# Optimization experiments

Measured on AMD Instinct MI355X. Metric: run time of the kernel, lower is better.

The kernel has to match this reference:

```python
import jax, jax.numpy as jnp
import numpy as np

D_FEATURE = 1024
HEAD = 16
D_K = 64
D_V = 64
EPS = 1e-6


def setup_inputs() -> dict:
    key = jax.random.key(0)
    ks = jax.random.split(key, 12)
    B, S = 2, 2048
    s_in = 1.0 / np.sqrt(D_FEATURE)
    s_o = 1.0 / np.sqrt(HEAD * D_V)
    return {
        "q": jax.random.normal(ks[0], (B, S, D_FEATURE), jnp.float32),
        "k": jax.random.normal(ks[1], (B, S, D_FEATURE), jnp.float32),
        "v": jax.random.normal(ks[2], (B, S, D_FEATURE), jnp.float32),
        "Wq": jax.random.uniform(ks[3], (D_FEATURE, HEAD * D_K), jnp.float32, -s_in, s_in),
        "bq": jnp.zeros((HEAD * D_K,), jnp.float32),
        "Wk": jax.random.uniform(ks[4], (D_FEATURE, HEAD * D_K), jnp.float32, -s_in, s_in),
        "bk": jnp.zeros((HEAD * D_K,), jnp.float32),
        "Wv": jax.random.uniform(ks[5], (D_FEATURE, HEAD * D_V), jnp.float32, -s_in, s_in),
        "bv": jnp.zeros((HEAD * D_V,), jnp.float32),
        "Wo": jax.random.uniform(ks[6], (HEAD * D_V, D_FEATURE), jnp.float32, -s_o, s_o),
        "bo": jnp.zeros((D_FEATURE,), jnp.float32),
        "gamma": jnp.ones((D_FEATURE,), jnp.float32),
        "beta": jnp.zeros((D_FEATURE,), jnp.float32),
    }


def reference(q, k, v, Wq, bq, Wk, bk, Wv, bv, Wo, bo, gamma, beta):
    B, Sq, _ = q.shape
    Sk, Sv = k.shape[1], v.shape[1]
    shortcut = v
    # projections -> (b, h, s, d)
    qh = (q @ Wq + bq).reshape(B, Sq, HEAD, D_K).transpose(0, 2, 1, 3)
    kh = (k @ Wk + bk).reshape(B, Sk, HEAD, D_K).transpose(0, 2, 1, 3)
    vh = (v @ Wv + bv).reshape(B, Sv, HEAD, D_V).transpose(0, 2, 1, 3)
    scale = 1.0 / np.sqrt(D_K).astype(np.float32)
    scores = jnp.einsum('bhqd,bhkd->bhqk', qh * scale, kh)
    attn = jax.nn.softmax(scores, axis=-1)  # dropout is identity (p=0 / eval)
    ctx = jnp.einsum('bhqk,bhkd->bhqd', attn, vh)
    ctx = ctx.transpose(0, 2, 1, 3).reshape(B, Sv, HEAD * D_V)
    out = ctx @ Wo + bo
    out = out + shortcut
    # LayerNorm, eps=1e-6
    mu = out.mean(-1, keepdims=True)
    var = out.var(-1, keepdims=True)
    out = (out - mu) * jax.lax.rsqrt(var + EPS) * gamma + beta
    return out
```

## Files before the change

### kernel.cpp

```cpp
#include <hip/hip_runtime.h>

#define D_FEAT 1024
#define NTOK   4096
#define SEQ    2048
#define NHEAD  16
#define DK     64
#define QSCALE 0.1803368801111204f

typedef float          f32x4  __attribute__((ext_vector_type(4)));
typedef float          f32x16 __attribute__((ext_vector_type(16)));
typedef short          s16x8  __attribute__((ext_vector_type(8)));
typedef unsigned short u16x4  __attribute__((ext_vector_type(4)));

__device__ __forceinline__ unsigned short f2bf(float f) {
  union { float f; unsigned int u; } x; x.f = f;
  unsigned int r = x.u + 0x7fffu + ((x.u >> 16) & 1u);
  return (unsigned short)(r >> 16);
}

__device__ __forceinline__ f32x4 mfma16(s16x8 a, s16x8 b, f32x4 c) {
  return __builtin_amdgcn_mfma_f32_16x16x32_bf16(a, b, c, 0, 0, 0);
}
__device__ __forceinline__ f32x16 mfma32(s16x8 a, s16x8 b, f32x16 c) {
  return __builtin_amdgcn_mfma_f32_32x32x16_bf16(a, b, c, 0, 0, 0);
}

__device__ __forceinline__ void gload16(const void* g, void* l) {
  __builtin_amdgcn_global_load_lds(
      (const __attribute__((address_space(1))) void*)g,
      (__attribute__((address_space(3))) void*)l, 16, 0, 0);
}

__global__ __launch_bounds__(256) void cast_bf16_kernel(
    const float* __restrict__ q, const float* __restrict__ k, const float* __restrict__ v,
    unsigned short* __restrict__ qb, unsigned short* __restrict__ kb, unsigned short* __restrict__ vb)
{
  int sel = blockIdx.y;
  const float* src = sel == 0 ? q : (sel == 1 ? k : v);
  unsigned short* dst = sel == 0 ? qb : (sel == 1 ? kb : vb);
  size_t i = ((size_t)blockIdx.x * 256 + threadIdx.x) * 4;
  float4 f = *(const float4*)(src + i);
  u16x4 o; o.x = f2bf(f.x); o.y = f2bf(f.y); o.z = f2bf(f.z); o.w = f2bf(f.w);
  *(u16x4*)(dst + i) = o;
}

__global__ __launch_bounds__(256) void transpose_cast_kernel(
    const float* __restrict__ W0, const float* __restrict__ W1,
    const float* __restrict__ W2, const float* __restrict__ W3,
    unsigned short* __restrict__ WT, unsigned short* __restrict__ Wot)
{
  __shared__ float tile[32][33];
  int z = blockIdx.z;
  const float* W = z == 0 ? W0 : z == 1 ? W1 : z == 2 ? W2 : W3;
  unsigned short* T = (z < 3) ? (WT + (size_t)z * 1024 * 1024) : Wot;
  int tx = threadIdx.x, ty = threadIdx.y;
  int n = blockIdx.x * 32 + tx;
  for (int i = 0; i < 4; ++i) {
    int k = blockIdx.y * 32 + ty + i * 8;
    tile[ty + i * 8][tx] = W[(size_t)k * D_FEAT + n];
  }
  __syncthreads();
  int k = blockIdx.y * 32 + tx;
  for (int i = 0; i < 4; ++i) {
    int n2 = blockIdx.x * 32 + ty + i * 8;
    T[(size_t)n2 * D_FEAT + k] = f2bf(tile[tx][ty + i * 8]);
  }
}

__global__ __launch_bounds__(256) void gemm_qkv(
    const unsigned short* __restrict__ qb, const unsigned short* __restrict__ kb,
    const unsigned short* __restrict__ vb, const unsigned short* __restrict__ WT,
    const float* __restrict__ bq, const float* __restrict__ bk, const float* __restrict__ bv,
    unsigned short* __restrict__ Qp, unsigned short* __restrict__ Kp, unsigned short* __restrict__ Vt)
{
  __shared__ __align__(16) unsigned short sA[128 * 32];
  __shared__ __align__(16) unsigned short sB[128 * 32];
  const int tid = threadIdx.x;
  const int wave = tid >> 6, lane = tid & 63;
  const int quad = lane >> 4, l16 = lane & 15;
  const int wx = wave & 1, wy = wave >> 1;
  const int bx = blockIdx.x;
  const int chunk = bx >> 3;

  const unsigned short* rA;
  const unsigned short* rB;
  int m0, n0;
  if (chunk < 2) {
    m0 = blockIdx.y * 128; n0 = (bx & 7) * 128;
    rA = (chunk ? kb : qb) + (size_t)m0 * D_FEAT;
    rB = WT + (size_t)(chunk * 1024 + n0) * D_FEAT;
  } else {
    m0 = (bx & 7) * 128; n0 = blockIdx.y * 128;
    rA = WT + (size_t)(2048 + m0) * D_FEAT;
    rB = vb + (size_t)n0 * D_FEAT;
  }

  f32x4 acc[4][4];
  for (int mt = 0; mt < 4; ++mt)
    for (int nt = 0; nt < 4; ++nt) acc[mt][nt] = (f32x4){0.f, 0.f, 0.f, 0.f};

  const int rw = lane >> 2;
  const int cl = (((lane & 3) ^ ((lane >> 3) & 3))) * 8;
  const int g0 = (quad ^ ((l16 >> 1) & 3)) * 8;

  for (int k0 = 0; k0 < D_FEAT; k0 += 32) {
    __syncthreads();
    for (int j = 0; j < 2; ++j) {
      int ch = wave * 2 + j;
      gload16(rA + (size_t)(ch * 16 + rw) * D_FEAT + k0 + cl, sA + ch * 512);
      gload16(rB + (size_t)(ch * 16 + rw) * D_FEAT + k0 + cl, sB + ch * 512);
    }
    __syncthreads();
    s16x8 af[4], bfr[4];
    for (int mt = 0; mt < 4; ++mt)
      af[mt] = *(const s16x8*)(sA + (wy * 64 + mt * 16 + l16) * 32 + g0);
    for (int nt = 0; nt < 4; ++nt)
      bfr[nt] = *(const s16x8*)(sB + (wx * 64 + nt * 16 + l16) * 32 + g0);
    for (int mt = 0; mt < 4; ++mt)
      for (int nt = 0; nt < 4; ++nt)
        acc[mt][nt] = mfma16(af[mt], bfr[nt], acc[mt][nt]);
  }

  if (chunk < 2) {
    const float* bias = chunk ? bk : bq;
    unsigned short* Cp = chunk ? Kp : Qp;
    const float scale = chunk == 0 ? QSCALE : 1.0f;
    for (int mt = 0; mt < 4; ++mt)
      for (int nt = 0; nt < 4; ++nt) {
        int col = n0 + wx * 64 + nt * 16 + l16;
        float bcol = bias[col];
        for (int r = 0; r < 4; ++r) {
          int row = m0 + wy * 64 + mt * 16 + quad * 4 + r;
          Cp[(size_t)row * D_FEAT + col] = f2bf((acc[mt][nt][r] + bcol) * scale);
        }
      }
  } else {
    for (int mt = 0; mt < 4; ++mt) {
      float bfeat[4];
      for (int r = 0; r < 4; ++r)
        bfeat[r] = bv[m0 + wy * 64 + mt * 16 + quad * 4 + r];
      for (int nt = 0; nt < 4; ++nt) {
        int n = n0 + wx * 64 + nt * 16 + l16;
        int b = n >> 11, tok = n & 2047;
        for (int r = 0; r < 4; ++r) {
          int f = m0 + wy * 64 + mt * 16 + quad * 4 + r;
          int h = f >> 6, dv = f & 63;
          Vt[(((size_t)(b * 16 + h) * 64 + dv) * SEQ) + tok] =
              f2bf(acc[mt][nt][r] + bfeat[r]);
        }
      }
    }
  }
}

__global__ __launch_bounds__(256) void gemm_o(
    const unsigned short* __restrict__ A, const unsigned short* __restrict__ Bt,
    const float* __restrict__ bias, const float* __restrict__ resid,
    float* __restrict__ Cout)
{
  __shared__ __align__(16) unsigned short sA[128 * 32];
  __shared__ __align__(16) unsigned short sB[64 * 32];
  const int tid = threadIdx.x;
  const int wave = tid >> 6, lane = tid & 63;
  const int quad = lane >> 4, l16 = lane & 15;
  const int wx = wave & 1, wy = wave >> 1;
  const int n0 = blockIdx.x * 64, m0 = blockIdx.y * 128;

  f32x4 acc[4][2];
  for (int mt = 0; mt < 4; ++mt)
    for (int nt = 0; nt < 2; ++nt) acc[mt][nt] = (f32x4){0.f, 0.f, 0.f, 0.f};

  const int rw = lane >> 2;
  const int cl = (((lane & 3) ^ ((lane >> 3) & 3))) * 8;
  const int g0 = (quad ^ ((l16 >> 1) & 3)) * 8;

  for (int k0 = 0; k0 < D_FEAT; k0 += 32) {
    __syncthreads();
    for (int j = 0; j < 2; ++j) {
      int ch = wave * 2 + j;
      gload16(A + (size_t)(m0 + ch * 16 + rw) * D_FEAT + k0 + cl, sA + ch * 512);
    }
    gload16(Bt + (size_t)(n0 + wave * 16 + rw) * D_FEAT + k0 + cl, sB + wave * 512);
    __syncthreads();
    s16x8 af[4], bfr[2];
    for (int mt = 0; mt < 4; ++mt)
      af[mt] = *(const s16x8*)(sA + (wy * 64 + mt * 16 + l16) * 32 + g0);
    for (int nt = 0; nt < 2; ++nt)
      bfr[nt] = *(const s16x8*)(sB + (wx * 32 + nt * 16 + l16) * 32 + g0);
    for (int mt = 0; mt < 4; ++mt)
      for (int nt = 0; nt < 2; ++nt)
        acc[mt][nt] = mfma16(af[mt], bfr[nt], acc[mt][nt]);
  }

  for (int mt = 0; mt < 4; ++mt)
    for (int nt = 0; nt < 2; ++nt) {
      int col = n0 + wx * 32 + nt * 16 + l16;
      float bcol = bias[col];
      for (int r = 0; r < 4; ++r) {
        int row = m0 + wy * 64 + mt * 16 + quad * 4 + r;
        Cout[(size_t)row * D_FEAT + col] =
            acc[mt][nt][r] + bcol + resid[(size_t)row * D_FEAT + col];
      }
    }
}

__global__ __launch_bounds__(256, 2) void flash_kernel(
    const unsigned short* __restrict__ Qp,
    const unsigned short* __restrict__ Kp,
    const unsigned short* __restrict__ Vt,
    unsigned short* __restrict__ ctx)
{
  __shared__ __align__(16) unsigned short sQ[128 * 64];
  __shared__ __align__(16) unsigned short sK[64 * 64];
  __shared__ __align__(16) unsigned short sV[64 * 64];

  const int tid = threadIdx.x;
  const int wave = tid >> 6, lane = tid & 63;
  const int l32 = lane & 31, h = lane >> 5;
  const int q0 = blockIdx.x * 128;
  const int bh = blockIdx.y, b = bh >> 4, hd = bh & 15;
  const size_t base = (size_t)b * SEQ * D_FEAT + (size_t)hd * DK;
  const unsigned short* vt = Vt + (size_t)bh * 64 * SEQ;

  const int rw8 = lane >> 3;
  const int cls = ((lane & 7) ^ (lane >> 3)) * 8;

  for (int j = 0; j < 4; ++j) {
    int ch = wave * 4 + j;
    gload16(Qp + base + (size_t)(q0 + ch * 8 + rw8) * D_FEAT + cls, sQ + ch * 512);
  }
  __syncthreads();

  const int qrow = wave * 32 + l32;
  const int qsw = qrow & 7;
  s16x8 bq[4];
  for (int s = 0; s < 4; ++s)
    bq[s] = *(const s16x8*)(sQ + qrow * 64 + ((2 * s + h) ^ qsw) * 8);

  unsigned short* sP = sQ;

  f32x16 o0, o1;
  for (int r = 0; r < 16; ++r) { o0[r] = 0.f; o1[r] = 0.f; }
  float m_i = -INFINITY, l_i = 0.f;

  const int ksw0 = l32 & 7;

  for (int k0 = 0; k0 < SEQ; k0 += 64) {
    __syncthreads();
    for (int j = 0; j < 2; ++j) {
      int ch = wave * 2 + j;
      gload16(Kp + base + (size_t)(k0 + ch * 8 + rw8) * D_FEAT + cls, sK + ch * 512);
      gload16(vt + (size_t)(ch * 8 + rw8) * SEQ + k0 + cls, sV + ch * 512);
    }
    __syncthreads();

    f32x16 st0, st1;
    for (int r = 0; r < 16; ++r) { st0[r] = 0.f; st1[r] = 0.f; }
    for (int s = 0; s < 4; ++s) {
      int csw = ((2 * s + h) ^ ksw0) * 8;
      s16x8 a0 = *(const s16x8*)(sK + l32 * 64 + csw);
      s16x8 a1 = *(const s16x8*)(sK + (32 + l32) * 64 + csw);
      st0 = mfma32(a0, bq[s], st0);
      st1 = mfma32(a1, bq[s], st1);
    }

    float mx = st0[0];
    for (int r = 0; r < 16; ++r) { mx = fmaxf(mx, st0[r]); mx = fmaxf(mx, st1[r]); }
    mx = fmaxf(mx, __shfl_xor(mx, 32, 64));
    float mn = fmaxf(m_i, mx);
    float alpha = __builtin_exp2f(m_i - mn);
    m_i = mn;

    float sum = 0.f;
    const int rowb = qrow * 64;
    for (int g = 0; g < 4; ++g) {
      unsigned int u[4];
      for (int r = 0; r < 4; ++r) {
        union { float f; unsigned int v; } x;
        x.f = __builtin_exp2f(st0[4 * g + r] - mn);
        sum += x.f; u[r] = x.v;
      }
      unsigned int w0 = __builtin_amdgcn_perm(u[1], u[0], 0x07060302u);
      unsigned int w1 = __builtin_amdgcn_perm(u[3], u[2], 0x07060302u);
      *(uint2*)(sP + rowb + ((g ^ qsw) * 8) + 4 * h) = make_uint2(w0, w1);
    }
    for (int g = 0; g < 4; ++g) {
      unsigned int u[4];
      for (int r = 0; r < 4; ++r) {
        union { float f; unsigned int v; } x;
        x.f = __builtin_exp2f(st1[4 * g + r] - mn);
        sum += x.f; u[r] = x.v;
      }
      unsigned int w0 = __builtin_amdgcn_perm(u[1], u[0], 0x07060302u);
      unsigned int w1 = __builtin_amdgcn_perm(u[3], u[2], 0x07060302u);
      *(uint2*)(sP + rowb + (((4 + g) ^ qsw) * 8) + 4 * h) = make_uint2(w0, w1);
    }
    sum += __shfl_xor(sum, 32, 64);
    l_i = l_i * alpha + sum;

    for (int r = 0; r < 16; ++r) { o0[r] *= alpha; o1[r] *= alpha; }

    s16x8 bp[4];
    for (int s = 0; s < 4; ++s)
      bp[s] = *(const s16x8*)(sP + rowb + ((2 * s + h) ^ qsw) * 8);

    for (int s = 0; s < 4; ++s) {
      int csw = ((2 * s + h) ^ ksw0) * 8;
      s16x8 a0 = *(const s16x8*)(sV + l32 * 64 + csw);
      s16x8 a1 = *(const s16x8*)(sV + (32 + l32) * 64 + csw);
      o0 = mfma32(a0, bp[s], o0);
      o1 = mfma32(a1, bp[s], o1);
    }
  }

  float inv = __builtin_amdgcn_rcpf(l_i);
  unsigned short* crow = ctx + base + (size_t)(q0 + qrow) * D_FEAT;
  for (int g = 0; g < 4; ++g) {
    u16x4 ov;
    for (int r = 0; r < 4; ++r) ov[r] = f2bf(o0[4 * g + r] * inv);
    *(u16x4*)(crow + 8 * g + 4 * h) = ov;
  }
  for (int g = 0; g < 4; ++g) {
    u16x4 ov;
    for (int r = 0; r < 4; ++r) ov[r] = f2bf(o1[4 * g + r] * inv);
    *(u16x4*)(crow + 32 + 8 * g + 4 * h) = ov;
  }
}

__global__ __launch_bounds__(256) void ln_kernel(
    const float* __restrict__ x, const float* __restrict__ gamma,
    const float* __restrict__ beta, float* __restrict__ out)
{
  const int row = blockIdx.x, tid = threadIdx.x;
  const int wave = tid >> 6, lane = tid & 63;
  const float* xr = x + (size_t)row * D_FEAT;
  float4 v = ((const float4*)xr)[tid];
  float s  = v.x + v.y + v.z + v.w;
  float ss = v.x * v.x + v.y * v.y + v.z * v.z + v.w * v.w;
  for (int off = 1; off < 64; off <<= 1) {
    s  += __shfl_xor(s,  off, 64);
    ss += __shfl_xor(ss, off, 64);
  }
  __shared__ float red[8];
  if (lane == 0) { red[wave] = s; red[wave + 4] = ss; }
  __syncthreads();
  s  = red[0] + red[1] + red[2] + red[3];
  ss = red[4] + red[5] + red[6] + red[7];
  float mean = s * (1.f / D_FEAT);
  float var  = ss * (1.f / D_FEAT) - mean * mean;
  float rstd = rsqrtf(var + 1e-6f);
  float4 g  = ((const float4*)gamma)[tid];
  float4 bt = ((const float4*)beta)[tid];
  float4 o;
  o.x = (v.x - mean) * rstd * g.x + bt.x;
  o.y = (v.y - mean) * rstd * g.y + bt.y;
  o.z = (v.z - mean) * rstd * g.z + bt.z;
  o.w = (v.w - mean) * rstd * g.w + bt.w;
  ((float4*)(out + (size_t)row * D_FEAT))[tid] = o;
}

extern "C" void kernel_launch(void* const* d_in, const int* in_sizes, int n_in,
                              void* d_out, int out_size, void* d_ws, size_t ws_size,
                              hipStream_t stream) {
  const float* q     = (const float*)d_in[0];
  const float* k     = (const float*)d_in[1];
  const float* v     = (const float*)d_in[2];
  const float* Wq    = (const float*)d_in[3];
  const float* bq    = (const float*)d_in[4];
  const float* Wk    = (const float*)d_in[5];
  const float* bk    = (const float*)d_in[6];
  const float* Wv    = (const float*)d_in[7];
  const float* bv    = (const float*)d_in[8];
  const float* Wo    = (const float*)d_in[9];
  const float* bo    = (const float*)d_in[10];
  const float* gamma = (const float*)d_in[11];
  const float* beta  = (const float*)d_in[12];

  char* w = (char*)d_ws;
  const size_t MB = 1u << 20;
  unsigned short* qb  = (unsigned short*)(w + 0 * MB);
  unsigned short* kb  = (unsigned short*)(w + 8 * MB);
  unsigned short* vb  = (unsigned short*)(w + 16 * MB);
  unsigned short* WT  = (unsigned short*)(w + 24 * MB);
  unsigned short* Wot = (unsigned short*)(w + 30 * MB);
  unsigned short* Qp  = (unsigned short*)(w + 32 * MB);
  unsigned short* Kp  = (unsigned short*)(w + 40 * MB);
  unsigned short* Vt  = (unsigned short*)(w + 48 * MB);
  unsigned short* ctx = (unsigned short*)(w + 56 * MB);
  float*          tmp = (float*)(w + 64 * MB);

  cast_bf16_kernel<<<dim3(4096, 3), 256, 0, stream>>>(q, k, v, qb, kb, vb);
  transpose_cast_kernel<<<dim3(32, 32, 4), dim3(32, 8), 0, stream>>>(
      Wq, Wk, Wv, Wo, WT, Wot);

  gemm_qkv<<<dim3(24, 32), 256, 0, stream>>>(qb, kb, vb, WT, bq, bk, bv, Qp, Kp, Vt);

  flash_kernel<<<dim3(SEQ / 128, 32), 256, 0, stream>>>(Qp, Kp, Vt, ctx);

  gemm_o<<<dim3(16, 32), 256, 0, stream>>>(ctx, Wot, bo, v, tmp);

  ln_kernel<<<NTOK, 256, 0, stream>>>(tmp, gamma, beta, (float*)d_out);
}
```

Measured before the change: 278.4 us.

## Split attention over key halves, merge prep kernels, widen GEMM K-tile

Several changes land together. The two preprocessing kernels are merged into one launch. Both GEMMs now use a 64-wide K tile with a new swizzle. The V projection epilogue transposes through LDS so it can write Vt with vectorized stores. Attention is split into two key-range halves per query block, which writes fp16 partial outputs plus max and sum statistics, and a new combine kernel merges them into ctx. The split doubles the flash grid for occupancy at the cost of an extra kernel and extra partial-output traffic; fp16 partials risk precision loss.

```diff
diff --git a/kernel.cpp b/kernel.cpp
--- a/kernel.cpp
+++ b/kernel.cpp
@@ -17,6 +17,12 @@
   unsigned int r = x.u + 0x7fffu + ((x.u >> 16) & 1u);
   return (unsigned short)(r >> 16);
 }
+__device__ __forceinline__ unsigned short f2h(float f) {
+  union { _Float16 h; unsigned short u; } x; x.h = (_Float16)f; return x.u;
+}
+__device__ __forceinline__ float h2f(unsigned short u) {
+  union { _Float16 h; unsigned short u; } x; x.u = u; return (float)x.h;
+}
 
 __device__ __forceinline__ f32x4 mfma16(s16x8 a, s16x8 b, f32x4 c) {
   return __builtin_amdgcn_mfma_f32_16x16x32_bf16(a, b, c, 0, 0, 0);
@@ -31,50 +37,54 @@
       (__attribute__((address_space(3))) void*)l, 16, 0, 0);
 }
 
-__global__ __launch_bounds__(256) void cast_bf16_kernel(
+__global__ __launch_bounds__(256) void prep_kernel(
     const float* __restrict__ q, const float* __restrict__ k, const float* __restrict__ v,
-    unsigned short* __restrict__ qb, unsigned short* __restrict__ kb, unsigned short* __restrict__ vb)
-{
-  int sel = blockIdx.y;
-  const float* src = sel == 0 ? q : (sel == 1 ? k : v);
-  unsigned short* dst = sel == 0 ? qb : (sel == 1 ? kb : vb);
-  size_t i = ((size_t)blockIdx.x * 256 + threadIdx.x) * 4;
-  float4 f = *(const float4*)(src + i);
-  u16x4 o; o.x = f2bf(f.x); o.y = f2bf(f.y); o.z = f2bf(f.z); o.w = f2bf(f.w);
-  *(u16x4*)(dst + i) = o;
-}
-
-__global__ __launch_bounds__(256) void transpose_cast_kernel(
-    const float* __restrict__ W0, const float* __restrict__ W1,
-    const float* __restrict__ W2, const float* __restrict__ W3,
+    const float* __restrict__ Wq, const float* __restrict__ Wk,
+    const float* __restrict__ Wv, const float* __restrict__ Wo,
+    unsigned short* __restrict__ qb, unsigned short* __restrict__ kb,
+    unsigned short* __restrict__ vb,
     unsigned short* __restrict__ WT, unsigned short* __restrict__ Wot)
 {
   __shared__ float tile[32][33];
-  int z = blockIdx.z;
-  const float* W = z == 0 ? W0 : z == 1 ? W1 : z == 2 ? W2 : W3;
-  unsigned short* T = (z < 3) ? (WT + (size_t)z * 1024 * 1024) : Wot;
-  int tx = threadIdx.x, ty = threadIdx.y;
-  int n = blockIdx.x * 32 + tx;
-  for (int i = 0; i < 4; ++i) {
-    int k = blockIdx.y * 32 + ty + i * 8;
-    tile[ty + i * 8][tx] = W[(size_t)k * D_FEAT + n];
-  }
-  __syncthreads();
-  int k = blockIdx.y * 32 + tx;
-  for (int i = 0; i < 4; ++i) {
-    int n2 = blockIdx.x * 32 + ty + i * 8;
-    T[(size_t)n2 * D_FEAT + k] = f2bf(tile[tx][ty + i * 8]);
-  }
-}
-
-__global__ __launch_bounds__(256) void gemm_qkv(
+  const int bx = blockIdx.x, tid = threadIdx.x;
+  if (bx < 12288) {
+    int sel = bx >> 12;
+    const float* src = sel == 0 ? q : (sel == 1 ? k : v);
+    unsigned short* dst = sel == 0 ? qb : (sel == 1 ? kb : vb);
+    size_t i = ((size_t)(bx & 4095) * 256 + tid) * 4;
+    float4 f = *(const float4*)(src + i);
+    u16x4 o; o.x = f2bf(f.x); o.y = f2bf(f.y); o.z = f2bf(f.z); o.w = f2bf(f.w);
+    *(u16x4*)(dst + i) = o;
+  } else {
+    int t = bx - 12288;
+    int z = t >> 10, rest = t & 1023;
+    int bxt = rest & 31, byt = rest >> 5;
+    const float* W = z == 0 ? Wq : z == 1 ? Wk : z == 2 ? Wv : Wo;
+    unsigned short* T = (z < 3) ? (WT + (size_t)z * 1024 * 1024) : Wot;
+    int tx = tid & 31, ty = tid >> 5;
+    int n = bxt * 32 + tx;
+    for (int i = 0; i < 4; ++i) {
+      int kk = byt * 32 + ty + i * 8;
+      tile[ty + i * 8][tx] = W[(size_t)kk * D_FEAT + n];
+    }
+    __syncthreads();
+    int kk = byt * 32 + tx;
+    for (int i = 0; i < 4; ++i) {
+      int n2 = bxt * 32 + ty + i * 8;
+      T[(size_t)n2 * D_FEAT + kk] = f2bf(tile[tx][ty + i * 8]);
+    }
+  }
+}
+
+__global__ __launch_bounds__(256, 3) void gemm_qkv(
     const unsigned short* __restrict__ qb, const unsigned short* __restrict__ kb,
     const unsigned short* __restrict__ vb, const unsigned short* __restrict__ WT,
     const float* __restrict__ bq, const float* __restrict__ bk, const float* __restrict__ bv,
     unsigned short* __restrict__ Qp, unsigned short* __restrict__ Kp, unsigned short* __restrict__ Vt)
 {
-  __shared__ __align__(16) unsigned short sA[128 * 32];
-  __shared__ __align__(16) unsigned short sB[128 * 32];
+  __shared__ __align__(16) unsigned short sAB[2 * 128 * 64];
+  unsigned short* sA = sAB;
+  unsigned short* sB = sAB + 128 * 64;
   const int tid = threadIdx.x;
   const int wave = tid >> 6, lane = tid & 63;
   const int quad = lane >> 4, l16 = lane & 15;
@@ -99,26 +109,30 @@
   for (int mt = 0; mt < 4; ++mt)
     for (int nt = 0; nt < 4; ++nt) acc[mt][nt] = (f32x4){0.f, 0.f, 0.f, 0.f};
 
-  const int rw = lane >> 2;
-  const int cl = (((lane & 3) ^ ((lane >> 3) & 3))) * 8;
-  const int g0 = (quad ^ ((l16 >> 1) & 3)) * 8;
-
-  for (int k0 = 0; k0 < D_FEAT; k0 += 32) {
-    __syncthreads();
-    for (int j = 0; j < 2; ++j) {
-      int ch = wave * 2 + j;
-      gload16(rA + (size_t)(ch * 16 + rw) * D_FEAT + k0 + cl, sA + ch * 512);
-      gload16(rB + (size_t)(ch * 16 + rw) * D_FEAT + k0 + cl, sB + ch * 512);
-    }
-    __syncthreads();
-    s16x8 af[4], bfr[4];
-    for (int mt = 0; mt < 4; ++mt)
-      af[mt] = *(const s16x8*)(sA + (wy * 64 + mt * 16 + l16) * 32 + g0);
-    for (int nt = 0; nt < 4; ++nt)
-      bfr[nt] = *(const s16x8*)(sB + (wx * 64 + nt * 16 + l16) * 32 + g0);
-    for (int mt = 0; mt < 4; ++mt)
+  const int rw8 = lane >> 3;
+  const int cls = ((lane & 7) ^ (lane >> 3)) * 8;
+  const int sw = l16 & 7;
+
+  for (int k0 = 0; k0 < D_FEAT; k0 += 64) {
+    __syncthreads();
+    for (int j = 0; j < 4; ++j) {
+      int ch = wave * 4 + j;
+      gload16(rA + (size_t)(ch * 8 + rw8) * D_FEAT + k0 + cls, sA + ch * 512);
+      gload16(rB + (size_t)(ch * 8 + rw8) * D_FEAT + k0 + cls, sB + ch * 512);
+    }
+    __syncthreads();
+    s16x8 af[2][4], bfr[2][4];
+    for (int kk = 0; kk < 2; ++kk) {
+      int c = ((kk * 4 + quad) ^ sw) * 8;
+      for (int mt = 0; mt < 4; ++mt)
+        af[kk][mt] = *(const s16x8*)(sA + (wy * 64 + mt * 16 + l16) * 64 + c);
       for (int nt = 0; nt < 4; ++nt)
-        acc[mt][nt] = mfma16(af[mt], bfr[nt], acc[mt][nt]);
+        bfr[kk][nt] = *(const s16x8*)(sB + (wx * 64 + nt * 16 + l16) * 64 + c);
+    }
+    for (int kk = 0; kk < 2; ++kk)
+      for (int mt = 0; mt < 4; ++mt)
+        for (int nt = 0; nt < 4; ++nt)
+          acc[mt][nt] = mfma16(af[kk][mt], bfr[kk][nt], acc[mt][nt]);
   }
 
   if (chunk < 2) {
@@ -135,19 +149,33 @@
         }
       }
   } else {
-    for (int mt = 0; mt < 4; ++mt) {
-      float bfeat[4];
-      for (int r = 0; r < 4; ++r)
-        bfeat[r] = bv[m0 + wy * 64 + mt * 16 + quad * 4 + r];
-      for (int nt = 0; nt < 4; ++nt) {
-        int n = n0 + wx * 64 + nt * 16 + l16;
-        int b = n >> 11, tok = n & 2047;
-        for (int r = 0; r < 4; ++r) {
-          int f = m0 + wy * 64 + mt * 16 + quad * 4 + r;
-          int h = f >> 6, dv = f & 63;
-          Vt[(((size_t)(b * 16 + h) * 64 + dv) * SEQ) + tok] =
-              f2bf(acc[mt][nt][r] + bfeat[r]);
-        }
+    for (int mt = 0; mt < 4; ++mt)
+      for (int r = 0; r < 4; ++r) {
+        float bfeat = bv[m0 + wy * 64 + mt * 16 + quad * 4 + r];
+        for (int nt = 0; nt < 4; ++nt) acc[mt][nt][r] += bfeat;
+      }
+    unsigned short* tb = sAB;
+    for (int p = 0; p < 2; ++p) {
+      __syncthreads();
+      if (wx == p) {
+        for (int mt = 0; mt < 4; ++mt)
+          for (int nt = 0; nt < 4; ++nt) {
+            int tok_loc = nt * 16 + l16;
+            for (int r = 0; r < 4; ++r) {
+              int f_loc = wy * 64 + mt * 16 + quad * 4 + r;
+              tb[f_loc * 72 + tok_loc] = f2bf(acc[mt][nt][r]);
+            }
+          }
+      }
+      __syncthreads();
+      int n_base = n0 + p * 64;
+      int b = n_base >> 11, tok0 = n_base & 2047;
+      int ck = lane & 7;
+      for (int j = 0; j < 4; ++j) {
+        int f_loc = (wave * 4 + j) * 8 + rw8;
+        int f = m0 + f_loc, hh = f >> 6, dv = f & 63;
+        *(s16x8*)(Vt + ((size_t)(b * 16 + hh) * 64 + dv) * SEQ + tok0 + ck * 8) =
+            *(const s16x8*)(tb + f_loc * 72 + ck * 8);
       }
     }
   }
@@ -158,8 +186,8 @@
     const float* __restrict__ bias, const float* __restrict__ resid,
     float* __restrict__ Cout)
 {
-  __shared__ __align__(16) unsigned short sA[128 * 32];
-  __shared__ __align__(16) unsigned short sB[64 * 32];
+  __shared__ __align__(16) unsigned short sA[128 * 64];
+  __shared__ __align__(16) unsigned short sB[64 * 64];
   const int tid = threadIdx.x;
   const int wave = tid >> 6, lane = tid & 63;
   const int quad = lane >> 4, l16 = lane & 15;
@@ -170,26 +198,33 @@
   for (int mt = 0; mt < 4; ++mt)
     for (int nt = 0; nt < 2; ++nt) acc[mt][nt] = (f32x4){0.f, 0.f, 0.f, 0.f};
 
-  const int rw = lane >> 2;
-  const int cl = (((lane & 3) ^ ((lane >> 3) & 3))) * 8;
-  const int g0 = (quad ^ ((l16 >> 1) & 3)) * 8;
-
-  for (int k0 = 0; k0 < D_FEAT; k0 += 32) {
-    __syncthreads();
+  const int rw8 = lane >> 3;
+  const int cls = ((lane & 7) ^ (lane >> 3)) * 8;
+  const int sw = l16 & 7;
+
+  for (int k0 = 0; k0 < D_FEAT; k0 += 64) {
+    __syncthreads();
+    for (int j = 0; j < 4; ++j) {
+      int ch = wave * 4 + j;
+      gload16(A + (size_t)(m0 + ch * 8 + rw8) * D_FEAT + k0 + cls, sA + ch * 512);
+    }
     for (int j = 0; j < 2; ++j) {
       int ch = wave * 2 + j;
-      gload16(A + (size_t)(m0 + ch * 16 + rw) * D_FEAT + k0 + cl, sA + ch * 512);
-    }
-    gload16(Bt + (size_t)(n0 + wave * 16 + rw) * D_FEAT + k0 + cl, sB + wave * 512);
-    __syncthreads();
-    s16x8 af[4], bfr[2];
-    for (int mt = 0; mt < 4; ++mt)
-      af[mt] = *(const s16x8*)(sA + (wy * 64 + mt * 16 + l16) * 32 + g0);
-    for (int nt = 0; nt < 2; ++nt)
-      bfr[nt] = *(const s16x8*)(sB + (wx * 32 + nt * 16 + l16) * 32 + g0);
-    for (int mt = 0; mt < 4; ++mt)
+      gload16(Bt + (size_t)(n0 + ch * 8 + rw8) * D_FEAT + k0 + cls, sB + ch * 512);
+    }
+    __syncthreads();
+    s16x8 af[2][4], bfr[2][2];
+    for (int kk = 0; kk < 2; ++kk) {
+      int c = ((kk * 4 + quad) ^ sw) * 8;
+      for (int mt = 0; mt < 4; ++mt)
+        af[kk][mt] = *(const s16x8*)(sA + (wy * 64 + mt * 16 + l16) * 64 + c);
       for (int nt = 0; nt < 2; ++nt)
-        acc[mt][nt] = mfma16(af[mt], bfr[nt], acc[mt][nt]);
+        bfr[kk][nt] = *(const s16x8*)(sB + (wx * 32 + nt * 16 + l16) * 64 + c);
+    }
+    for (int kk = 0; kk < 2; ++kk)
+      for (int mt = 0; mt < 4; ++mt)
+        for (int nt = 0; nt < 2; ++nt)
+          acc[mt][nt] = mfma16(af[kk][mt], bfr[kk][nt], acc[mt][nt]);
   }
 
   for (int mt = 0; mt < 4; ++mt)
@@ -204,11 +239,12 @@
     }
 }
 
-__global__ __launch_bounds__(256, 2) void flash_kernel(
+__global__ __launch_bounds__(256, 4) void flash_part(
     const unsigned short* __restrict__ Qp,
     const unsigned short* __restrict__ Kp,
     const unsigned short* __restrict__ Vt,
-    unsigned short* __restrict__ ctx)
+    unsigned short* __restrict__ Opart,
+    float2* __restrict__ Ml)
 {
   __shared__ __align__(16) unsigned short sQ[128 * 64];
   __shared__ __align__(16) unsigned short sK[64 * 64];
@@ -219,6 +255,8 @@
   const int l32 = lane & 31, h = lane >> 5;
   const int q0 = blockIdx.x * 128;
   const int bh = blockIdx.y, b = bh >> 4, hd = bh & 15;
+  const int z = blockIdx.z;
+  const int kbase = z * (SEQ / 2);
   const size_t base = (size_t)b * SEQ * D_FEAT + (size_t)hd * DK;
   const unsigned short* vt = Vt + (size_t)bh * 64 * SEQ;
 
@@ -245,7 +283,7 @@
 
   const int ksw0 = l32 & 7;
 
-  for (int k0 = 0; k0 < SEQ; k0 += 64) {
+  for (int k0 = kbase; k0 < kbase + SEQ / 2; k0 += 64) {
     __syncthreads();
     for (int j = 0; j < 2; ++j) {
       int ch = wave * 2 + j;
@@ -313,18 +351,43 @@
     }
   }
 
-  float inv = __builtin_amdgcn_rcpf(l_i);
-  unsigned short* crow = ctx + base + (size_t)(q0 + qrow) * D_FEAT;
+  const size_t trow = (size_t)(z * 32 + bh) * SEQ + (q0 + qrow);
+  unsigned short* orow = Opart + trow * 64;
   for (int g = 0; g < 4; ++g) {
     u16x4 ov;
-    for (int r = 0; r < 4; ++r) ov[r] = f2bf(o0[4 * g + r] * inv);
-    *(u16x4*)(crow + 8 * g + 4 * h) = ov;
+    for (int r = 0; r < 4; ++r) ov[r] = f2h(o0[4 * g + r]);
+    *(u16x4*)(orow + 8 * g + 4 * h) = ov;
   }
   for (int g = 0; g < 4; ++g) {
     u16x4 ov;
-    for (int r = 0; r < 4; ++r) ov[r] = f2bf(o1[4 * g + r] * inv);
-    *(u16x4*)(crow + 32 + 8 * g + 4 * h) = ov;
-  }
+    for (int r = 0; r < 4; ++r) ov[r] = f2h(o1[4 * g + r]);
+    *(u16x4*)(orow + 32 + 8 * g + 4 * h) = ov;
+  }
+  if (h == 0) Ml[trow] = make_float2(m_i, l_i);
+}
+
+__global__ __launch_bounds__(256) void combine_kernel(
+    const unsigned short* __restrict__ Opart, const float2* __restrict__ Ml,
+    unsigned short* __restrict__ ctx)
+{
+  const int idx = blockIdx.x * 256 + threadIdx.x;
+  const int dq = idx & 15;
+  const int trow = idx >> 4;
+  const int bh = trow >> 11, tok = trow & 2047;
+  const int b = bh >> 4, h = bh & 15;
+  const int HS = 32 * SEQ;
+
+  float2 ml0 = Ml[trow], ml1 = Ml[HS + trow];
+  float m = fmaxf(ml0.x, ml1.x);
+  float w0 = __builtin_exp2f(ml0.x - m), w1 = __builtin_exp2f(ml1.x - m);
+  float inv = __builtin_amdgcn_rcpf(ml0.y * w0 + ml1.y * w1);
+
+  u16x4 p0 = *(const u16x4*)(Opart + (size_t)trow * 64 + dq * 4);
+  u16x4 p1 = *(const u16x4*)(Opart + ((size_t)HS + trow) * 64 + dq * 4);
+  u16x4 o;
+  for (int r = 0; r < 4; ++r)
+    o[r] = f2bf((h2f(p0[r]) * w0 + h2f(p1[r]) * w1) * inv);
+  *(u16x4*)(ctx + (size_t)b * SEQ * D_FEAT + (size_t)tok * D_FEAT + h * 64 + dq * 4) = o;
 }
 
 __global__ __launch_bounds__(256) void ln_kernel(
@@ -378,24 +441,26 @@
 
   char* w = (char*)d_ws;
   const size_t MB = 1u << 20;
-  unsigned short* qb  = (unsigned short*)(w + 0 * MB);
-  unsigned short* kb  = (unsigned short*)(w + 8 * MB);
-  unsigned short* vb  = (unsigned short*)(w + 16 * MB);
-  unsigned short* WT  = (unsigned short*)(w + 24 * MB);
-  unsigned short* Wot = (unsigned short*)(w + 30 * MB);
-  unsigned short* Qp  = (unsigned short*)(w + 32 * MB);
-  unsigned short* Kp  = (unsigned short*)(w + 40 * MB);
-  unsigned short* Vt  = (unsigned short*)(w + 48 * MB);
-  unsigned short* ctx = (unsigned short*)(w + 56 * MB);
-  float*          tmp = (float*)(w + 64 * MB);
-
-  cast_bf16_kernel<<<dim3(4096, 3), 256, 0, stream>>>(q, k, v, qb, kb, vb);
-  transpose_cast_kernel<<<dim3(32, 32, 4), dim3(32, 8), 0, stream>>>(
-      Wq, Wk, Wv, Wo, WT, Wot);
+  unsigned short* qb    = (unsigned short*)(w + 0 * MB);
+  unsigned short* kb    = (unsigned short*)(w + 8 * MB);
+  unsigned short* vb    = (unsigned short*)(w + 16 * MB);
+  unsigned short* WT    = (unsigned short*)(w + 24 * MB);
+  unsigned short* Wot   = (unsigned short*)(w + 30 * MB);
+  unsigned short* Qp    = (unsigned short*)(w + 32 * MB);
+  unsigned short* Kp    = (unsigned short*)(w + 40 * MB);
+  unsigned short* Vt    = (unsigned short*)(w + 48 * MB);
+  unsigned short* ctx   = (unsigned short*)(w + 56 * MB);
+  float*          tmp   = (float*)(w + 64 * MB);
+  unsigned short* Opart = (unsigned short*)(w + 0 * MB);
+  float2*         Ml    = (float2*)(w + 16 * MB);
+
+  prep_kernel<<<16384, 256, 0, stream>>>(q, k, v, Wq, Wk, Wv, Wo, qb, kb, vb, WT, Wot);
 
   gemm_qkv<<<dim3(24, 32), 256, 0, stream>>>(qb, kb, vb, WT, bq, bk, bv, Qp, Kp, Vt);
 
-  flash_kernel<<<dim3(SEQ / 128, 32), 256, 0, stream>>>(Qp, Kp, Vt, ctx);
+  flash_part<<<dim3(SEQ / 128, 32, 2), 256, 0, stream>>>(Qp, Kp, Vt, Opart, Ml);
+
+  combine_kernel<<<4096, 256, 0, stream>>>(Opart, Ml, ctx);
 
   gemm_o<<<dim3(16, 32), 256, 0, stream>>>(ctx, Wot, bo, v, tmp);
 
```

Measured after the change: 254.1 us. 1.1x faster.
